# Performance work log

Measured on AMD Instinct MI355X. Metric: run time of the kernel, lower is better.

The kernel has to match this reference:

```python
import jax, jax.numpy as jnp
import numpy as np

TOP_K = 8
NUM_EXPERTS = 128
HIDDEN = 2048
TOKENS = 16384
NORM_TOPK_PROB = True


def setup_inputs() -> dict:
    key = jax.random.key(0)
    k1, k2 = jax.random.split(key)
    hidden_states = jax.random.normal(k1, (TOKENS, HIDDEN), dtype=jnp.float32)
    # gate weight [num_experts, hidden] (nn.Linear layout)
    weight = jax.random.normal(k2, (NUM_EXPERTS, HIDDEN), dtype=jnp.float32) * 0.02
    return {"hidden_states": hidden_states, "weight": weight}


def reference(hidden_states, weight):
    x = hidden_states.reshape(-1, HIDDEN)
    # router_logits: [tokens, num_experts]
    router_logits = jnp.einsum("td,ed->te", x, weight)
    router_probs = jax.nn.softmax(router_logits.astype(jnp.float32), axis=-1)
    top_vals, top_idx = jax.lax.top_k(router_probs, TOP_K)
    if NORM_TOPK_PROB:
        top_vals = top_vals / jnp.sum(top_vals, axis=-1, keepdims=True)
    top_vals = top_vals.astype(hidden_states.dtype)
    return router_logits, top_vals, top_idx
```

## Files before the change

### kernel.cpp

```cpp
#include <hip/hip_runtime.h>
#include <float.h>
#include <math.h>

#define TOKENS 16384
#define HIDDEN 2048
#define NEXP 128
#define TOPK 8
#define NCAND 12
#define DELTA 1e-3f

#define BM 64
#define BN 64
#define BK 64

typedef float f32x4 __attribute__((ext_vector_type(4)));
typedef short bf16x8 __attribute__((ext_vector_type(8)));

__device__ __forceinline__ unsigned pack_hi(float a, float b) {
    return (__float_as_uint(a) >> 16) | (__float_as_uint(b) & 0xFFFF0000u);
}
__device__ __forceinline__ float resid(float a) {
    return a - __uint_as_float(__float_as_uint(a) & 0xFFFF0000u);
}

__device__ __forceinline__ int ldsIdx(int mt, int kc, int hl, int lane) {
    return (((mt * 2 + kc) * 2 + hl) * 64 + lane) * 8;
}

__global__ __launch_bounds__(256) void router_gemm(const float* __restrict__ X,
                                                   const float* __restrict__ W,
                                                   float* __restrict__ logits) {
    __shared__ unsigned short sA[4 * 2 * 2 * 64 * 8];
    __shared__ unsigned short sB[4 * 2 * 2 * 64 * 8];

    const int tid = threadIdx.x;
    const int lane = tid & 63;
    const int wid = tid >> 6;
    const int wm = wid & 1, wn = wid >> 1;
    const int t0 = (blockIdx.x >> 1) * BM;
    const int e0 = (blockIdx.x & 1) * BN;

    const int xt = tid >> 2;
    const int xq = tid & 3;
    const int kc0 = xq >> 1;
    const int g0 = (xq * 2) & 3;
    const int m15 = xt & 15;
    const int mtile = xt >> 4;
    const int offH0 = ldsIdx(mtile, kc0, 0, g0 * 16 + m15);
    const int offH1 = ldsIdx(mtile, kc0, 0, (g0 + 1) * 16 + m15);
    const int offL0 = ldsIdx(mtile, kc0, 1, g0 * 16 + m15);
    const int offL1 = ldsIdx(mtile, kc0, 1, (g0 + 1) * 16 + m15);

    const float* Xp = X + (size_t)(t0 + xt) * HIDDEN + xq * 16;
    const float* Wp = W + (size_t)(e0 + xt) * HIDDEN + xq * 16;

    f32x4 acc[2][2];
#pragma unroll
    for (int i = 0; i < 2; ++i)
#pragma unroll
        for (int j = 0; j < 2; ++j) acc[i][j] = (f32x4){0.f, 0.f, 0.f, 0.f};

    float4 px[4], pw[4];
#pragma unroll
    for (int i = 0; i < 4; ++i) {
        px[i] = *(const float4*)(Xp + i * 4);
        pw[i] = *(const float4*)(Wp + i * 4);
    }

#pragma unroll 1
    for (int kt = 0; kt < HIDDEN; kt += BK) {
        __syncthreads();
        {
            uint4 h, l;
            h.x = pack_hi(px[0].x, px[0].y); h.y = pack_hi(px[0].z, px[0].w);
            h.z = pack_hi(px[1].x, px[1].y); h.w = pack_hi(px[1].z, px[1].w);
            l.x = pack_hi(resid(px[0].x), resid(px[0].y));
            l.y = pack_hi(resid(px[0].z), resid(px[0].w));
            l.z = pack_hi(resid(px[1].x), resid(px[1].y));
            l.w = pack_hi(resid(px[1].z), resid(px[1].w));
            *(uint4*)&sA[offH0] = h; *(uint4*)&sA[offL0] = l;
            h.x = pack_hi(px[2].x, px[2].y); h.y = pack_hi(px[2].z, px[2].w);
            h.z = pack_hi(px[3].x, px[3].y); h.w = pack_hi(px[3].z, px[3].w);
            l.x = pack_hi(resid(px[2].x), resid(px[2].y));
            l.y = pack_hi(resid(px[2].z), resid(px[2].w));
            l.z = pack_hi(resid(px[3].x), resid(px[3].y));
            l.w = pack_hi(resid(px[3].z), resid(px[3].w));
            *(uint4*)&sA[offH1] = h; *(uint4*)&sA[offL1] = l;

            h.x = pack_hi(pw[0].x, pw[0].y); h.y = pack_hi(pw[0].z, pw[0].w);
            h.z = pack_hi(pw[1].x, pw[1].y); h.w = pack_hi(pw[1].z, pw[1].w);
            l.x = pack_hi(resid(pw[0].x), resid(pw[0].y));
            l.y = pack_hi(resid(pw[0].z), resid(pw[0].w));
            l.z = pack_hi(resid(pw[1].x), resid(pw[1].y));
            l.w = pack_hi(resid(pw[1].z), resid(pw[1].w));
            *(uint4*)&sB[offH0] = h; *(uint4*)&sB[offL0] = l;
            h.x = pack_hi(pw[2].x, pw[2].y); h.y = pack_hi(pw[2].z, pw[2].w);
            h.z = pack_hi(pw[3].x, pw[3].y); h.w = pack_hi(pw[3].z, pw[3].w);
            l.x = pack_hi(resid(pw[2].x), resid(pw[2].y));
            l.y = pack_hi(resid(pw[2].z), resid(pw[2].w));
            l.z = pack_hi(resid(pw[3].x), resid(pw[3].y));
            l.w = pack_hi(resid(pw[3].z), resid(pw[3].w));
            *(uint4*)&sB[offH1] = h; *(uint4*)&sB[offL1] = l;
        }
        __syncthreads();

        if (kt + BK < HIDDEN) {
#pragma unroll
            for (int i = 0; i < 4; ++i) {
                px[i] = *(const float4*)(Xp + kt + BK + i * 4);
                pw[i] = *(const float4*)(Wp + kt + BK + i * 4);
            }
        }

#pragma unroll
        for (int kc = 0; kc < 2; ++kc) {
            bf16x8 ah[2], al[2], bh[2], bl[2];
#pragma unroll
            for (int mt = 0; mt < 2; ++mt) {
                ah[mt] = *(const bf16x8*)&sA[ldsIdx(wm * 2 + mt, kc, 0, lane)];
                al[mt] = *(const bf16x8*)&sA[ldsIdx(wm * 2 + mt, kc, 1, lane)];
            }
#pragma unroll
            for (int nt = 0; nt < 2; ++nt) {
                bh[nt] = *(const bf16x8*)&sB[ldsIdx(wn * 2 + nt, kc, 0, lane)];
                bl[nt] = *(const bf16x8*)&sB[ldsIdx(wn * 2 + nt, kc, 1, lane)];
            }
#pragma unroll
            for (int mt = 0; mt < 2; ++mt)
#pragma unroll
                for (int nt = 0; nt < 2; ++nt) {
                    acc[mt][nt] = __builtin_amdgcn_mfma_f32_16x16x32_bf16(ah[mt], bh[nt], acc[mt][nt], 0, 0, 0);
                    acc[mt][nt] = __builtin_amdgcn_mfma_f32_16x16x32_bf16(ah[mt], bl[nt], acc[mt][nt], 0, 0, 0);
                    acc[mt][nt] = __builtin_amdgcn_mfma_f32_16x16x32_bf16(al[mt], bh[nt], acc[mt][nt], 0, 0, 0);
                }
        }
    }

#pragma unroll
    for (int mt = 0; mt < 2; ++mt) {
        const int tr = t0 + wm * 32 + mt * 16 + (lane >> 4) * 4;
#pragma unroll
        for (int nt = 0; nt < 2; ++nt) {
            const int ec = e0 + wn * 32 + nt * 16 + (lane & 15);
#pragma unroll
            for (int r = 0; r < 4; ++r)
                logits[(size_t)(tr + r) * NEXP + ec] = acc[mt][nt][r];
        }
    }
}

__device__ __forceinline__ void top_cand(const float* __restrict__ lrow, int lane,
                                         float* vals, int* idxs) {
    const float l0 = lrow[lane];
    const float l1 = lrow[lane + 64];
    bool r0 = false, r1 = false;
#pragma unroll
    for (int it = 0; it < NCAND; ++it) {
        const float c0 = r0 ? -FLT_MAX : l0;
        const float c1 = r1 ? -FLT_MAX : l1;
        float v; int id;
        if (c1 > c0) { v = c1; id = lane + 64; }
        else         { v = c0; id = lane; }
#pragma unroll
        for (int off = 1; off < 64; off <<= 1) {
            const float ov = __shfl_xor(v, off);
            const int   oi = __shfl_xor(id, off);
            if (ov > v || (ov == v && oi < id)) { v = ov; id = oi; }
        }
        vals[it] = v; idxs[it] = id;
        if (id == lane) r0 = true;
        else if (id == lane + 64) r1 = true;
    }
}

__global__ __launch_bounds__(256) void router_select(const float* __restrict__ logits,
                                                     float* __restrict__ top_vals,
                                                     float* __restrict__ top_idx,
                                                     int* __restrict__ cnt,
                                                     int* __restrict__ list) {
    const int lane = threadIdx.x & 63;
    const int wid = threadIdx.x >> 6;
    const int t = blockIdx.x * 4 + wid;

    float vals[NCAND]; int idxs[NCAND];
    top_cand(logits + (size_t)t * NEXP, lane, vals, idxs);

    float ming = FLT_MAX;
#pragma unroll
    for (int i = 0; i < TOPK; ++i) ming = fminf(ming, vals[i] - vals[i + 1]);

    if (ming < DELTA) {
        if (lane == 0) { const int p = atomicAdd(cnt, 1); list[p] = t; }
    } else if (lane == 0) {
        const float m = vals[0];
        float e[TOPK], s = 0.f;
#pragma unroll
        for (int i = 0; i < TOPK; ++i) { e[i] = expf(vals[i] - m); s += e[i]; }
        const float inv = 1.f / s;
#pragma unroll
        for (int i = 0; i < TOPK; ++i) {
            top_vals[(size_t)t * TOPK + i] = e[i] * inv;
            top_idx[(size_t)t * TOPK + i] = (float)idxs[i];
        }
    }
}

__global__ __launch_bounds__(256) void router_refine(const float* __restrict__ logits,
                                                     const float* __restrict__ X,
                                                     const float* __restrict__ W,
                                                     float* __restrict__ top_vals,
                                                     float* __restrict__ top_idx,
                                                     const int* __restrict__ cnt,
                                                     const int* __restrict__ list) {
    const int lane = threadIdx.x & 63;
    const int gw = blockIdx.x * 4 + (threadIdx.x >> 6);
    const int nwaves = gridDim.x * 4;
    const int n = *cnt;

    for (int ii = gw; ii < n; ii += nwaves) {
        const int t = list[ii];
        float vals[NCAND]; int idxs[NCAND];
        top_cand(logits + (size_t)t * NEXP, lane, vals, idxs);

        const float* xr = X + (size_t)t * HIDDEN;
        double xd[32];
#pragma unroll
        for (int j = 0; j < 8; ++j) {
            const float4 v = *(const float4*)(xr + j * 256 + lane * 4);
            xd[j * 4 + 0] = (double)v.x; xd[j * 4 + 1] = (double)v.y;
            xd[j * 4 + 2] = (double)v.z; xd[j * 4 + 3] = (double)v.w;
        }
        double acc[NCAND];
#pragma unroll
        for (int c = 0; c < NCAND; ++c) {
            const float* wr = W + (size_t)idxs[c] * HIDDEN;
            double a0 = 0.0, a1 = 0.0;
#pragma unroll
            for (int j = 0; j < 8; ++j) {
                const float4 w = *(const float4*)(wr + j * 256 + lane * 4);
                a0 = fma((double)w.x, xd[j * 4 + 0], a0);
                a1 = fma((double)w.y, xd[j * 4 + 1], a1);
                a0 = fma((double)w.z, xd[j * 4 + 2], a0);
                a1 = fma((double)w.w, xd[j * 4 + 3], a1);
            }
            acc[c] = a0 + a1;
        }
#pragma unroll
        for (int c = 0; c < NCAND; ++c)
#pragma unroll
            for (int off = 1; off < 64; off <<= 1)
                acc[c] += __shfl_xor(acc[c], off);

        int rank[NCAND];
#pragma unroll
        for (int c = 0; c < NCAND; ++c) {
            int r = 0;
#pragma unroll
            for (int m = 0; m < NCAND; ++m)
                if (acc[m] > acc[c] || (acc[m] == acc[c] && idxs[m] < idxs[c])) ++r;
            rank[c] = r;
        }
        double vmax = acc[0];
#pragma unroll
        for (int c = 0; c < NCAND; ++c) if (rank[c] == 0) vmax = acc[c];
        float e[NCAND], s = 0.f;
#pragma unroll
        for (int c = 0; c < NCAND; ++c) {
            e[c] = (rank[c] < TOPK) ? expf((float)(acc[c] - vmax)) : 0.f;
            s += e[c];
        }
        const float inv = 1.f / s;
        if (lane == 0) {
#pragma unroll
            for (int c = 0; c < NCAND; ++c)
                if (rank[c] < TOPK) {
                    top_vals[(size_t)t * TOPK + rank[c]] = e[c] * inv;
                    top_idx[(size_t)t * TOPK + rank[c]] = (float)idxs[c];
                }
        }
    }
}

extern "C" void kernel_launch(void* const* d_in, const int* in_sizes, int n_in,
                              void* d_out, int out_size, void* d_ws, size_t ws_size,
                              hipStream_t stream) {
    const float* X = (const float*)d_in[0];
    const float* W = (const float*)d_in[1];
    float* logits = (float*)d_out;
    float* tvals  = logits + (size_t)TOKENS * NEXP;
    float* tidx   = tvals + (size_t)TOKENS * TOPK;
    int* cnt  = (int*)d_ws;
    int* list = (int*)d_ws + 16;

    hipMemsetAsync(d_ws, 0, 64, stream);
    router_gemm<<<(TOKENS / BM) * (NEXP / BN), 256, 0, stream>>>(X, W, logits);
    router_select<<<TOKENS / 4, 256, 0, stream>>>(logits, tvals, tidx, cnt, list);
    router_refine<<<256, 256, 0, stream>>>(logits, X, W, tvals, tidx, cnt, list);
}
```

Measured before the change: 294.2 us.

## Presplit W to bf16 hi/lo, double-buffer GEMM with direct LDS loads, thread-per-token select

Adds a kernel that splits W into bf16 hi/lo once per call in an MFMA-friendly layout. The GEMM now gives each block a 32-token strip across all 128 experts, so X is read once and not converted twice. W tiles go straight into double-buffered LDS via global_load_lds with a swizzled A layout, which removes one barrier per iteration and overlaps loads with compute. The wave-per-token shuffle top-k becomes a thread-per-token insertion sort over an LDS-staged row. Costs are an extra kernel launch, a workspace copy of W, and a serial 128-step select loop per thread.

```diff
diff --git a/kernel.cpp b/kernel.cpp
--- a/kernel.cpp
+++ b/kernel.cpp
@@ -7,11 +7,12 @@
 #define NEXP 128
 #define TOPK 8
 #define NCAND 12
+#define NSEL 13
 #define DELTA 1e-3f
 
-#define BM 64
-#define BN 64
-#define BK 64
+#define BM 32
+#define BK 32
+#define KITERS (HIDDEN / BK)
 
 typedef float f32x4 __attribute__((ext_vector_type(4)));
 typedef short bf16x8 __attribute__((ext_vector_type(8)));
@@ -22,129 +23,185 @@
 __device__ __forceinline__ float resid(float a) {
     return a - __uint_as_float(__float_as_uint(a) & 0xFFFF0000u);
 }
-
-__device__ __forceinline__ int ldsIdx(int mt, int kc, int hl, int lane) {
-    return (((mt * 2 + kc) * 2 + hl) * 64 + lane) * 8;
+__device__ __forceinline__ unsigned short hi16(float a) {
+    return (unsigned short)(__float_as_uint(a) >> 16);
+}
+
+__device__ __forceinline__ void load_lds_16B(const void* g, void* l) {
+    __builtin_amdgcn_global_load_lds(
+        (const __attribute__((address_space(1))) unsigned int*)g,
+        (__attribute__((address_space(3))) unsigned int*)l, 16, 0, 0);
+}
+
+__global__ __launch_bounds__(256) void presplit_w(const float* __restrict__ W,
+                                                  unsigned short* __restrict__ Ws) {
+    const int c = blockIdx.x * 256 + threadIdx.x;
+    const int lane = c & 63;
+    const int reg = (c >> 6) & 15;
+    const int kt = c >> 10;
+    const int nt = reg >> 1, hl = reg & 1;
+    const int e = nt * 16 + (lane & 15);
+    const int k0 = kt * 32 + (lane >> 4) * 8;
+    const float* wp = W + (size_t)e * HIDDEN + k0;
+    float4 a = *(const float4*)wp;
+    float4 b = *(const float4*)(wp + 4);
+    if (hl) {
+        a.x = resid(a.x); a.y = resid(a.y); a.z = resid(a.z); a.w = resid(a.w);
+        b.x = resid(b.x); b.y = resid(b.y); b.z = resid(b.z); b.w = resid(b.w);
+    }
+    uint4 o;
+    o.x = pack_hi(a.x, a.y); o.y = pack_hi(a.z, a.w);
+    o.z = pack_hi(b.x, b.y); o.w = pack_hi(b.z, b.w);
+    *(uint4*)(Ws + (size_t)c * 8) = o;
 }
 
 __global__ __launch_bounds__(256) void router_gemm(const float* __restrict__ X,
-                                                   const float* __restrict__ W,
+                                                   const unsigned short* __restrict__ Ws,
                                                    float* __restrict__ logits) {
-    __shared__ unsigned short sA[4 * 2 * 2 * 64 * 8];
-    __shared__ unsigned short sB[4 * 2 * 2 * 64 * 8];
-
+    __shared__ unsigned short sA[2][2 * 2 * 512];
+    __shared__ unsigned short sB[2][16 * 512];
     const int tid = threadIdx.x;
     const int lane = tid & 63;
     const int wid = tid >> 6;
     const int wm = wid & 1, wn = wid >> 1;
-    const int t0 = (blockIdx.x >> 1) * BM;
-    const int e0 = (blockIdx.x & 1) * BN;
-
-    const int xt = tid >> 2;
-    const int xq = tid & 3;
-    const int kc0 = xq >> 1;
-    const int g0 = (xq * 2) & 3;
-    const int m15 = xt & 15;
-    const int mtile = xt >> 4;
-    const int offH0 = ldsIdx(mtile, kc0, 0, g0 * 16 + m15);
-    const int offH1 = ldsIdx(mtile, kc0, 0, (g0 + 1) * 16 + m15);
-    const int offL0 = ldsIdx(mtile, kc0, 1, g0 * 16 + m15);
-    const int offL1 = ldsIdx(mtile, kc0, 1, (g0 + 1) * 16 + m15);
-
-    const float* Xp = X + (size_t)(t0 + xt) * HIDDEN + xq * 16;
-    const float* Wp = W + (size_t)(e0 + xt) * HIDDEN + xq * 16;
-
-    f32x4 acc[2][2];
-#pragma unroll
-    for (int i = 0; i < 2; ++i)
-#pragma unroll
-        for (int j = 0; j < 2; ++j) acc[i][j] = (f32x4){0.f, 0.f, 0.f, 0.f};
-
-    float4 px[4], pw[4];
-#pragma unroll
-    for (int i = 0; i < 4; ++i) {
-        px[i] = *(const float4*)(Xp + i * 4);
-        pw[i] = *(const float4*)(Wp + i * 4);
-    }
+    const int t0 = blockIdx.x * BM;
+
+    const int arow = tid >> 3, aq = tid & 7;
+    const int ag = aq >> 1, ar = arow & 15, am = arow >> 4;
+    const int aoff = (ag * 16 + (ar ^ ag)) * 8 + (aq & 1) * 4;
+    const int aH = (am * 2 + 0) * 512 + aoff;
+    const int aL = (am * 2 + 1) * 512 + aoff;
+    const float* Xp = X + (size_t)(t0 + arow) * HIDDEN + aq * 4;
+
+    const int rg = lane >> 4, rr = lane & 15;
+    const int aRd = (rg * 16 + (rr ^ rg)) * 8;
+
+    f32x4 acc[4];
+#pragma unroll
+    for (int nt = 0; nt < 4; ++nt) acc[nt] = (f32x4){0.f, 0.f, 0.f, 0.f};
+
+    {
+        const unsigned short* src = Ws + wid * 512 + lane * 8;
+        unsigned short* dst = &sB[0][wid * 512];
+        load_lds_16B(src, dst);
+        load_lds_16B(src + 2048, dst + 2048);
+        load_lds_16B(src + 4096, dst + 4096);
+        load_lds_16B(src + 6144, dst + 6144);
+        const float4 v = *(const float4*)(Xp);
+        ushort4 h, l;
+        h.x = hi16(v.x); h.y = hi16(v.y); h.z = hi16(v.z); h.w = hi16(v.w);
+        l.x = hi16(resid(v.x)); l.y = hi16(resid(v.y));
+        l.z = hi16(resid(v.z)); l.w = hi16(resid(v.w));
+        *(ushort4*)&sA[0][aH] = h;
+        *(ushort4*)&sA[0][aL] = l;
+    }
+    float4 xv = *(const float4*)(Xp + 32);
+    __syncthreads();
 
 #pragma unroll 1
-    for (int kt = 0; kt < HIDDEN; kt += BK) {
+    for (int kt = 0; kt < KITERS; ++kt) {
+        const int b = kt & 1;
+        if (kt + 1 < KITERS) {
+            const unsigned short* src = Ws + (size_t)(kt + 1) * 8192 + wid * 512 + lane * 8;
+            unsigned short* dst = &sB[b ^ 1][wid * 512];
+            load_lds_16B(src, dst);
+            load_lds_16B(src + 2048, dst + 2048);
+            load_lds_16B(src + 4096, dst + 4096);
+            load_lds_16B(src + 6144, dst + 6144);
+            ushort4 h, l;
+            h.x = hi16(xv.x); h.y = hi16(xv.y); h.z = hi16(xv.z); h.w = hi16(xv.w);
+            l.x = hi16(resid(xv.x)); l.y = hi16(resid(xv.y));
+            l.z = hi16(resid(xv.z)); l.w = hi16(resid(xv.w));
+            *(ushort4*)&sA[b ^ 1][aH] = h;
+            *(ushort4*)&sA[b ^ 1][aL] = l;
+        }
+        if (kt + 2 < KITERS) xv = *(const float4*)(Xp + (kt + 2) * 32);
+
+        const bf16x8 ah = *(const bf16x8*)&sA[b][(wm * 2 + 0) * 512 + aRd];
+        const bf16x8 al = *(const bf16x8*)&sA[b][(wm * 2 + 1) * 512 + aRd];
+#pragma unroll
+        for (int nt = 0; nt < 4; ++nt) {
+            const int rb = ((wn * 4 + nt) * 2) * 512 + lane * 8;
+            const bf16x8 bh = *(const bf16x8*)&sB[b][rb];
+            const bf16x8 bl = *(const bf16x8*)&sB[b][rb + 512];
+            acc[nt] = __builtin_amdgcn_mfma_f32_16x16x32_bf16(ah, bh, acc[nt], 0, 0, 0);
+            acc[nt] = __builtin_amdgcn_mfma_f32_16x16x32_bf16(ah, bl, acc[nt], 0, 0, 0);
+            acc[nt] = __builtin_amdgcn_mfma_f32_16x16x32_bf16(al, bh, acc[nt], 0, 0, 0);
+        }
         __syncthreads();
-        {
-            uint4 h, l;
-            h.x = pack_hi(px[0].x, px[0].y); h.y = pack_hi(px[0].z, px[0].w);
-            h.z = pack_hi(px[1].x, px[1].y); h.w = pack_hi(px[1].z, px[1].w);
-            l.x = pack_hi(resid(px[0].x), resid(px[0].y));
-            l.y = pack_hi(resid(px[0].z), resid(px[0].w));
-            l.z = pack_hi(resid(px[1].x), resid(px[1].y));
-            l.w = pack_hi(resid(px[1].z), resid(px[1].w));
-            *(uint4*)&sA[offH0] = h; *(uint4*)&sA[offL0] = l;
-            h.x = pack_hi(px[2].x, px[2].y); h.y = pack_hi(px[2].z, px[2].w);
-            h.z = pack_hi(px[3].x, px[3].y); h.w = pack_hi(px[3].z, px[3].w);
-            l.x = pack_hi(resid(px[2].x), resid(px[2].y));
-            l.y = pack_hi(resid(px[2].z), resid(px[2].w));
-            l.z = pack_hi(resid(px[3].x), resid(px[3].y));
-            l.w = pack_hi(resid(px[3].z), resid(px[3].w));
-            *(uint4*)&sA[offH1] = h; *(uint4*)&sA[offL1] = l;
-
-            h.x = pack_hi(pw[0].x, pw[0].y); h.y = pack_hi(pw[0].z, pw[0].w);
-            h.z = pack_hi(pw[1].x, pw[1].y); h.w = pack_hi(pw[1].z, pw[1].w);
-            l.x = pack_hi(resid(pw[0].x), resid(pw[0].y));
-            l.y = pack_hi(resid(pw[0].z), resid(pw[0].w));
-            l.z = pack_hi(resid(pw[1].x), resid(pw[1].y));
-            l.w = pack_hi(resid(pw[1].z), resid(pw[1].w));
-            *(uint4*)&sB[offH0] = h; *(uint4*)&sB[offL0] = l;
-            h.x = pack_hi(pw[2].x, pw[2].y); h.y = pack_hi(pw[2].z, pw[2].w);
-            h.z = pack_hi(pw[3].x, pw[3].y); h.w = pack_hi(pw[3].z, pw[3].w);
-            l.x = pack_hi(resid(pw[2].x), resid(pw[2].y));
-            l.y = pack_hi(resid(pw[2].z), resid(pw[2].w));
-            l.z = pack_hi(resid(pw[3].x), resid(pw[3].y));
-            l.w = pack_hi(resid(pw[3].z), resid(pw[3].w));
-            *(uint4*)&sB[offH1] = h; *(uint4*)&sB[offL1] = l;
-        }
-        __syncthreads();
-
-        if (kt + BK < HIDDEN) {
-#pragma unroll
-            for (int i = 0; i < 4; ++i) {
-                px[i] = *(const float4*)(Xp + kt + BK + i * 4);
-                pw[i] = *(const float4*)(Wp + kt + BK + i * 4);
+    }
+
+    const int tr = t0 + wm * 16 + (lane >> 4) * 4;
+    const int ec0 = lane & 15;
+#pragma unroll
+    for (int nt = 0; nt < 4; ++nt) {
+        const int e = (wn * 4 + nt) * 16 + ec0;
+#pragma unroll
+        for (int r = 0; r < 4; ++r)
+            logits[(size_t)(tr + r) * NEXP + e] = acc[nt][r];
+    }
+}
+
+__global__ __launch_bounds__(64) void router_select(const float* __restrict__ logits,
+                                                    float* __restrict__ top_vals,
+                                                    float* __restrict__ top_idx,
+                                                    int* __restrict__ cnt,
+                                                    int* __restrict__ list) {
+    __shared__ float Ls[64 * 133];
+    const int tid = threadIdx.x;
+    const int t0 = blockIdx.x * 64;
+#pragma unroll
+    for (int i = 0; i < 32; ++i) {
+        const int idx = i * 64 + tid;
+        const int row = idx >> 5, c4 = (idx & 31) * 4;
+        const float4 v = *(const float4*)(logits + (size_t)(t0 + row) * NEXP + c4);
+        float* d = &Ls[row * 133 + c4];
+        d[0] = v.x; d[1] = v.y; d[2] = v.z; d[3] = v.w;
+    }
+    __syncthreads();
+
+    const float* Lr = &Ls[tid * 133];
+    float vals[NSEL]; int idxs[NSEL];
+#pragma unroll
+    for (int j = 0; j < NSEL; ++j) { vals[j] = -FLT_MAX; idxs[j] = 0; }
+    for (int e = 0; e < NEXP; ++e) {
+        const float v = Lr[e];
+        if (v > vals[NSEL - 1]) {
+            int r = 0;
+#pragma unroll
+            for (int j = 0; j < NSEL; ++j) r += (vals[j] >= v) ? 1 : 0;
+#pragma unroll
+            for (int j = NSEL - 1; j > 0; --j) {
+                const bool c = (j > r);
+                vals[j] = c ? vals[j - 1] : vals[j];
+                idxs[j] = c ? idxs[j - 1] : idxs[j];
             }
-        }
-
-#pragma unroll
-        for (int kc = 0; kc < 2; ++kc) {
-            bf16x8 ah[2], al[2], bh[2], bl[2];
-#pragma unroll
-            for (int mt = 0; mt < 2; ++mt) {
-                ah[mt] = *(const bf16x8*)&sA[ldsIdx(wm * 2 + mt, kc, 0, lane)];
-                al[mt] = *(const bf16x8*)&sA[ldsIdx(wm * 2 + mt, kc, 1, lane)];
+#pragma unroll
+            for (int j = 0; j < NSEL; ++j) {
+                const bool c = (j == r);
+                vals[j] = c ? v : vals[j];
+                idxs[j] = c ? e : idxs[j];
             }
-#pragma unroll
-            for (int nt = 0; nt < 2; ++nt) {
-                bh[nt] = *(const bf16x8*)&sB[ldsIdx(wn * 2 + nt, kc, 0, lane)];
-                bl[nt] = *(const bf16x8*)&sB[ldsIdx(wn * 2 + nt, kc, 1, lane)];
-            }
-#pragma unroll
-            for (int mt = 0; mt < 2; ++mt)
-#pragma unroll
-                for (int nt = 0; nt < 2; ++nt) {
-                    acc[mt][nt] = __builtin_amdgcn_mfma_f32_16x16x32_bf16(ah[mt], bh[nt], acc[mt][nt], 0, 0, 0);
-                    acc[mt][nt] = __builtin_amdgcn_mfma_f32_16x16x32_bf16(ah[mt], bl[nt], acc[mt][nt], 0, 0, 0);
-                    acc[mt][nt] = __builtin_amdgcn_mfma_f32_16x16x32_bf16(al[mt], bh[nt], acc[mt][nt], 0, 0, 0);
-                }
-        }
-    }
-
-#pragma unroll
-    for (int mt = 0; mt < 2; ++mt) {
-        const int tr = t0 + wm * 32 + mt * 16 + (lane >> 4) * 4;
-#pragma unroll
-        for (int nt = 0; nt < 2; ++nt) {
-            const int ec = e0 + wn * 32 + nt * 16 + (lane & 15);
-#pragma unroll
-            for (int r = 0; r < 4; ++r)
-                logits[(size_t)(tr + r) * NEXP + ec] = acc[mt][nt][r];
+        }
+    }
+
+    const int t = t0 + tid;
+    float ming = FLT_MAX;
+#pragma unroll
+    for (int i = 0; i < TOPK; ++i) ming = fminf(ming, vals[i] - vals[i + 1]);
+    if (ming < DELTA) {
+        const int p = atomicAdd(cnt, 1);
+        list[p] = t;
+    } else {
+        const float m = vals[0];
+        float ex[TOPK], s = 0.f;
+#pragma unroll
+        for (int i = 0; i < TOPK; ++i) { ex[i] = expf(vals[i] - m); s += ex[i]; }
+        const float inv = 1.f / s;
+#pragma unroll
+        for (int i = 0; i < TOPK; ++i) {
+            top_vals[(size_t)t * TOPK + i] = ex[i] * inv;
+            top_idx[(size_t)t * TOPK + i] = (float)idxs[i];
         }
     }
 }
@@ -170,38 +227,6 @@
         vals[it] = v; idxs[it] = id;
         if (id == lane) r0 = true;
         else if (id == lane + 64) r1 = true;
-    }
-}
-
-__global__ __launch_bounds__(256) void router_select(const float* __restrict__ logits,
-                                                     float* __restrict__ top_vals,
-                                                     float* __restrict__ top_idx,
-                                                     int* __restrict__ cnt,
-                                                     int* __restrict__ list) {
-    const int lane = threadIdx.x & 63;
-    const int wid = threadIdx.x >> 6;
-    const int t = blockIdx.x * 4 + wid;
-
-    float vals[NCAND]; int idxs[NCAND];
-    top_cand(logits + (size_t)t * NEXP, lane, vals, idxs);
-
-    float ming = FLT_MAX;
-#pragma unroll
-    for (int i = 0; i < TOPK; ++i) ming = fminf(ming, vals[i] - vals[i + 1]);
-
-    if (ming < DELTA) {
-        if (lane == 0) { const int p = atomicAdd(cnt, 1); list[p] = t; }
-    } else if (lane == 0) {
-        const float m = vals[0];
-        float e[TOPK], s = 0.f;
-#pragma unroll
-        for (int i = 0; i < TOPK; ++i) { e[i] = expf(vals[i] - m); s += e[i]; }
-        const float inv = 1.f / s;
-#pragma unroll
-        for (int i = 0; i < TOPK; ++i) {
-            top_vals[(size_t)t * TOPK + i] = e[i] * inv;
-            top_idx[(size_t)t * TOPK + i] = (float)idxs[i];
-        }
     }
 }
 
@@ -289,11 +314,14 @@
     float* logits = (float*)d_out;
     float* tvals  = logits + (size_t)TOKENS * NEXP;
     float* tidx   = tvals + (size_t)TOKENS * TOPK;
-    int* cnt  = (int*)d_ws;
-    int* list = (int*)d_ws + 16;
+
+    int* cnt = (int*)d_ws;
+    unsigned short* Wsplit = (unsigned short*)((char*)d_ws + 4096);
+    int* list = (int*)((char*)d_ws + 4096 + 2 * 1024 * 1024);
 
     hipMemsetAsync(d_ws, 0, 64, stream);
-    router_gemm<<<(TOKENS / BM) * (NEXP / BN), 256, 0, stream>>>(X, W, logits);
-    router_select<<<TOKENS / 4, 256, 0, stream>>>(logits, tvals, tidx, cnt, list);
+    presplit_w<<<256, 256, 0, stream>>>(W, Wsplit);
+    router_gemm<<<TOKENS / BM, 256, 0, stream>>>(X, Wsplit, logits);
+    router_select<<<TOKENS / 64, 64, 0, stream>>>(logits, tvals, tidx, cnt, list);
     router_refine<<<256, 256, 0, stream>>>(logits, X, W, tvals, tidx, cnt, list);
 }
```

After: 324.8 us. 1.1x slower.
